# Kernel optimization log

Hardware: AMD Instinct MI355X
Metric: run time of the kernel (lower is better)

Reference implementation:

```python
import jax, jax.numpy as jnp
import numpy as np

N = 50000
E = 800000
NFEAT = 128
NHID = 64
NCLASS = 40


def setup_inputs() -> dict:
    key = jax.random.key(0)
    ks = jax.random.split(key, 12)
    return {
        "x": jax.random.normal(ks[0], (N, NFEAT), dtype=jnp.float32),
        "M": jax.random.uniform(ks[1], (N, 1), dtype=jnp.float32),
        "AM": jax.random.uniform(ks[2], (N, 1), dtype=jnp.float32),
        "adj_vals": jax.random.uniform(ks[3], (E,), dtype=jnp.float32),
        "adjZ_vals": jax.random.uniform(ks[4], (E,), dtype=jnp.float32),
        "W0": jax.random.normal(ks[5], (NFEAT, NFEAT), dtype=jnp.float32) * (1.414 / np.sqrt(NFEAT)),
        "b0": jnp.zeros((NFEAT,), dtype=jnp.float32),
        "W1": jax.random.normal(ks[6], (NFEAT, NHID), dtype=jnp.float32) * (1.414 / np.sqrt(NFEAT)),
        "b1": jnp.zeros((NHID,), dtype=jnp.float32),
        "W2": jax.random.normal(ks[7], (NHID, NCLASS), dtype=jnp.float32) * (1.0 / np.sqrt(NHID)),
        "b2": jnp.zeros((NCLASS,), dtype=jnp.float32),
        "row": jax.random.randint(ks[8], (E,), 0, N, dtype=jnp.int32),
        "col": jax.random.randint(ks[9], (E,), 0, N, dtype=jnp.int32),
    }


def _spmm(vals, row, col, X, n):
    # sparse (COO) @ dense: out[r] = sum_e vals[e] * X[col[e]] for row[e]==r
    return jax.ops.segment_sum(vals[:, None] * X[col], row, num_segments=n)


def reference(x, M, AM, adj_vals, adjZ_vals, W0, b0, W1, b1, W2, b2, row, col):
    n = x.shape[0]
    # gc0: PaGConv(nfeat->nfeat) on adjZ, then ReLU (dropout is identity in eval)
    h = _spmm(adjZ_vals, row, col, M * x, n) * AM
    h = jax.nn.relu(h @ W0 + b0)
    # gc1: PaGConv(nfeat->nhid) on adjZ, then ReLU
    h = _spmm(adjZ_vals, row, col, M * h, n) * AM
    h = jax.nn.relu(h @ W1 + b1)
    # gc2: plain GConv(nhid->nclass) on adj
    h = _spmm(adj_vals, row, col, h, n)
    h = h @ W2 + b2
    return jax.nn.log_softmax(h, axis=1)
```

## Files before the change

kernel.cpp:

```cpp
#include <hip/hip_runtime.h>
#include <hip/hip_bf16.h>
#include <math.h>


typedef __attribute__((ext_vector_type(8))) short bf16x8;
typedef __attribute__((ext_vector_type(4))) float f32x4;

#define HIST_EPB_LOG 14
#define HIST_EPB 16384
#define NBINS 50176
#define NBMAX 50
#define SCAN_BLOCKS 196

__device__ __forceinline__ float rl_f(float v, int j) {
    return __builtin_bit_cast(float,
        __builtin_amdgcn_readlane(__builtin_bit_cast(int, v), j));
}
__device__ __forceinline__ int rl_i(int v, int j) {
    return __builtin_amdgcn_readlane(v, j);
}
__device__ __forceinline__ unsigned short f2bf(float f) {
    unsigned u = __builtin_bit_cast(unsigned, f);
    u += 0x7fffu + ((u >> 16) & 1u);
    return (unsigned short)(u >> 16);
}
__device__ __forceinline__ unsigned pack2bf(float lo, float hi) {
    return (unsigned)f2bf(lo) | ((unsigned)f2bf(hi) << 16);
}
__device__ __forceinline__ float bf_lo(unsigned u) {
    return __builtin_bit_cast(float, u << 16);
}
__device__ __forceinline__ float bf_hi(unsigned u) {
    return __builtin_bit_cast(float, u & 0xffff0000u);
}
__device__ __forceinline__ float clampf(float v) {
    return fminf(fmaxf(v, -1e30f), 1e30f);
}
__device__ __forceinline__ unsigned long long aload(const unsigned long long* p) {
    return __hip_atomic_load(p, __ATOMIC_ACQUIRE, __HIP_MEMORY_SCOPE_AGENT);
}


__global__ void prep_wt(const float* __restrict__ W0, const float* __restrict__ W1,
                        const float* __restrict__ W2,
                        unsigned short* __restrict__ wt0, unsigned short* __restrict__ wt1,
                        unsigned short* __restrict__ wt2,
                        unsigned long long* __restrict__ gpub) {
    if (blockIdx.x == 0) gpub[threadIdx.x] = 0ULL;
    int idx = blockIdx.x * 256 + threadIdx.x;
    if (idx < 128 * 128) {
        int nn = idx >> 7, k = idx & 127;
        wt0[idx] = f2bf(W0[k * 128 + nn]);
    }
    idx -= 128 * 128;
    if (idx >= 0 && idx < 64 * 128) {
        int nn = idx >> 7, k = idx & 127;
        wt1[idx] = f2bf(W1[k * 64 + nn]);
    }
    idx -= 64 * 128;
    if (idx >= 0 && idx < 48 * 64) {
        int nn = idx >> 6, k = idx & 63;
        wt2[idx] = (nn < 40) ? f2bf(W2[k * 40 + nn]) : (unsigned short)0;
    }
}


__launch_bounds__(1024)
__global__ void hist_gemm0(const int* __restrict__ row,
                           unsigned short* __restrict__ cntmat,
                           unsigned short* __restrict__ lrank, int E, int NB,
                           const float* __restrict__ x, const float* __restrict__ Mv,
                           const unsigned short* __restrict__ Wt0,
                           unsigned short* __restrict__ t_buf, int n) {
    __shared__ __align__(16) unsigned hcnt[NBINS / 2];
    const int blk = blockIdx.x;
    const int t = threadIdx.x;
    if (blk < NB) {
        uint4* h4 = (uint4*)hcnt;
        const uint4 z4 = make_uint4(0u, 0u, 0u, 0u);
        for (int i = t; i < NBINS / 8; i += 1024) h4[i] = z4;
        __syncthreads();
        const int s = blk << HIST_EPB_LOG;
        const int e = min(E, s + HIST_EPB);
        for (int i = s + t; i < e; i += 1024) {
            const int r = row[i];
            const unsigned sh = (unsigned)(r & 1) << 4;
            const unsigned old = atomicAdd(&hcnt[r >> 1], 1u << sh);
            lrank[i] = (unsigned short)((old >> sh) & 0xffffu);
        }
        __syncthreads();
        uint4* dst = (uint4*)(cntmat + (size_t)blk * NBINS);
        for (int i = t; i < NBINS / 8; i += 1024) dst[i] = h4[i];
    } else {
        const int tid = t & 255;
        const int bid = (blk - NB) * 4 + (t >> 8);
        const int lane = tid & 63;
        const int wid = tid >> 6;
        const int m15 = lane & 15;
        const int q = lane >> 4;
        const int rA = bid * 64 + wid * 16 + m15;

        bf16x8 a[4];
        {
            float m = 1.0f;
            if (rA < n) m = Mv[rA];
#pragma unroll
            for (int ks = 0; ks < 4; ++ks) {
                float4 lo = make_float4(0.f, 0.f, 0.f, 0.f);
                float4 hi = make_float4(0.f, 0.f, 0.f, 0.f);
                if (rA < n) {
                    lo = *(const float4*)(x + (size_t)rA * 128 + ks * 32 + q * 8);
                    hi = *(const float4*)(x + (size_t)rA * 128 + ks * 32 + q * 8 + 4);
                }
                union { bf16x8 v; unsigned short u[8]; } pk;
                pk.u[0] = f2bf(lo.x * m); pk.u[1] = f2bf(lo.y * m);
                pk.u[2] = f2bf(lo.z * m); pk.u[3] = f2bf(lo.w * m);
                pk.u[4] = f2bf(hi.x * m); pk.u[5] = f2bf(hi.y * m);
                pk.u[6] = f2bf(hi.z * m); pk.u[7] = f2bf(hi.w * m);
                a[ks] = pk.v;
            }
        }
#pragma unroll
        for (int nt = 0; nt < 8; ++nt) {
            f32x4 acc = {0.f, 0.f, 0.f, 0.f};
            const int bn = nt * 16 + m15;
#pragma unroll
            for (int ks = 0; ks < 4; ++ks) {
                const uint4 z = *(const uint4*)(Wt0 + (size_t)bn * 128 + ks * 32 + q * 8);
                acc = __builtin_amdgcn_mfma_f32_16x16x32_bf16(
                    a[ks], __builtin_bit_cast(bf16x8, z), acc, 0, 0, 0);
            }
            const int gc = nt * 16 + m15;
#pragma unroll
            for (int rr = 0; rr < 4; ++rr) {
                const int gr = bid * 64 + wid * 16 + q * 4 + rr;
                if (gr < n) t_buf[(size_t)gr * 128 + gc] = f2bf(clampf(acc[rr]));
            }
        }
    }
}


__launch_bounds__(256)
__global__ void scan_one(const unsigned short* __restrict__ cm,
                         unsigned* __restrict__ cmabs, int* __restrict__ rp,
                         unsigned long long* __restrict__ gpub,
                         int n, int NB, int E) {
    __shared__ int sd[256];
    const int g = blockIdx.x;
    const int t = threadIdx.x;
    const int bin = g * 256 + t;

    unsigned tot = 0;
    for (int b = 0; b < NB; ++b) tot += cm[(size_t)b * NBINS + bin];

    sd[t] = (int)tot;
    __syncthreads();
    for (int off = 1; off < 256; off <<= 1) {
        int xv = (t >= off) ? sd[t - off] : 0;
        __syncthreads();
        sd[t] += xv;
        __syncthreads();
    }
    const int excl = sd[t] - (int)tot;
    const int gtot = sd[255];
    __syncthreads();

    if (t == 0)
        atomicExch(&gpub[g], (1ULL << 32) | (unsigned long long)(unsigned)gtot);

    int my = 0;
    for (int p = t; p < g; p += 256) {
        unsigned long long v;
        do { v = aload(&gpub[p]); } while ((v >> 32) == 0ULL);
        my += (int)(unsigned)v;
    }
    sd[t] = my;
    __syncthreads();
    for (int off = 128; off > 0; off >>= 1) {
        if (t < off) sd[t] += sd[t + off];
        __syncthreads();
    }
    const int base = sd[0];

    const int rpf = base + excl;
    if (bin < n) rp[bin] = rpf;
    if (g == SCAN_BLOCKS - 1 && t == 255) rp[n] = E;

    int run = rpf;
    for (int b = 0; b < NB; ++b) {
        cmabs[(size_t)b * NBINS + bin] = (unsigned)run;
        run += (int)cm[(size_t)b * NBINS + bin];
    }
}


__global__ void scatter_kernel(const int* __restrict__ row, const int* __restrict__ col,
                               const float* __restrict__ vA, const float* __restrict__ vZ,
                               const unsigned* __restrict__ cmabs,
                               const unsigned short* __restrict__ lrank,
                               uint4* __restrict__ packed16, int E) {
    int e = blockIdx.x * blockDim.x + threadIdx.x;
    if (e >= E) return;
    const int r = row[e];
    const int pos = (int)(cmabs[(size_t)(e >> HIST_EPB_LOG) * NBINS + r]
                          + (unsigned)lrank[e]);
    uint4 pk;
    pk.x = (unsigned)col[e];
    pk.y = __builtin_bit_cast(unsigned, vZ[e]);
    pk.z = __builtin_bit_cast(unsigned, vA[e]);
    pk.w = 0u;
    packed16[pos] = pk;
}


__launch_bounds__(256)
__global__ void spmm128_g1(const uint4* __restrict__ packed16,
                           const int* __restrict__ rp, const unsigned short* __restrict__ X,
                           const float* __restrict__ AM, const float* __restrict__ Mv,
                           const float* __restrict__ bias,
                           const unsigned short* __restrict__ wt1,
                           unsigned short* __restrict__ g1, int n) {
    __shared__ __align__(16) unsigned short h16[16][136];
    const int t = threadIdx.x;
    const int lane = t & 63;
    const int w = t >> 6;
    const int rbase = blockIdx.x * 16;

    for (int i = 0; i < 4; ++i) {
        const int lr = w * 4 + i;
        const int r = rbase + lr;
        float o0 = 0.0f, o1 = 0.0f;
        if (r < n) {
            const int s = __builtin_amdgcn_readfirstlane(rp[r]);
            const int e = __builtin_amdgcn_readfirstlane(rp[r + 1]);
            float acc0 = 0.0f, acc1 = 0.0f;
            for (int base = s; base < e; base += 64) {
                const int nn = min(64, e - base);
                int ci = 0; float vf = 0.0f;
                if (lane < nn) {
                    const uint4 pk = packed16[base + lane];
                    ci = (int)pk.x;
                    vf = __builtin_bit_cast(float, pk.y);
                }
                int j = 0;
                for (; j + 16 <= nn; j += 16) {
                    unsigned u[16];
#pragma unroll
                    for (int q = 0; q < 16; ++q) {
                        const int cq = rl_i(ci, j + q);
                        u[q] = *(const unsigned*)(X + (size_t)cq * 128 + lane * 2);
                    }
#pragma unroll
                    for (int q = 0; q < 16; ++q) {
                        const float vq = rl_f(vf, j + q);
                        acc0 += vq * bf_lo(u[q]);
                        acc1 += vq * bf_hi(u[q]);
                    }
                }
                for (; j + 8 <= nn; j += 8) {
                    unsigned u[8];
#pragma unroll
                    for (int q = 0; q < 8; ++q) {
                        const int cq = rl_i(ci, j + q);
                        u[q] = *(const unsigned*)(X + (size_t)cq * 128 + lane * 2);
                    }
#pragma unroll
                    for (int q = 0; q < 8; ++q) {
                        const float vq = rl_f(vf, j + q);
                        acc0 += vq * bf_lo(u[q]);
                        acc1 += vq * bf_hi(u[q]);
                    }
                }
                for (; j < nn; ++j) {
                    const int cq = rl_i(ci, j);
                    const float vq = rl_f(vf, j);
                    const unsigned u = *(const unsigned*)(X + (size_t)cq * 128 + lane * 2);
                    acc0 += vq * bf_lo(u);
                    acc1 += vq * bf_hi(u);
                }
            }
            const float am = AM[r];
            const float mr = Mv[r];
            o0 = fminf(fmaxf((acc0 * am + bias[2 * lane]) * mr, 0.0f), 1e30f);
            o1 = fminf(fmaxf((acc1 * am + bias[2 * lane + 1]) * mr, 0.0f), 1e30f);
        }
        *(unsigned*)&h16[lr][2 * lane] = pack2bf(o0, o1);
    }
    __syncthreads();

    const int m15 = lane & 15;
    const int q = lane >> 4;
    bf16x8 a[4];
#pragma unroll
    for (int ks = 0; ks < 4; ++ks)
        a[ks] = __builtin_bit_cast(bf16x8,
                    *(const uint4*)&h16[m15][ks * 32 + q * 8]);
    f32x4 acc = {0.f, 0.f, 0.f, 0.f};
    const int bn = w * 16 + m15;
#pragma unroll
    for (int ks = 0; ks < 4; ++ks) {
        const uint4 z = *(const uint4*)(wt1 + (size_t)bn * 128 + ks * 32 + q * 8);
        acc = __builtin_amdgcn_mfma_f32_16x16x32_bf16(
            a[ks], __builtin_bit_cast(bf16x8, z), acc, 0, 0, 0);
    }
    const int gcol = w * 16 + m15;
#pragma unroll
    for (int rr = 0; rr < 4; ++rr) {
        const int grow = rbase + q * 4 + rr;
        if (grow < n) g1[(size_t)grow * 64 + gcol] = f2bf(clampf(acc[rr]));
    }
}


__launch_bounds__(256)
__global__ void spmm64_g2(const uint4* __restrict__ packed16,
                          const int* __restrict__ rp, const unsigned short* __restrict__ X,
                          const float* __restrict__ AM, const float* __restrict__ bias1,
                          const unsigned short* __restrict__ wt2,
                          unsigned short* __restrict__ out40, int n) {
    __shared__ __align__(16) unsigned short h16[16][72];
    const int t = threadIdx.x;
    const int lane = t & 63;
    const int w = t >> 6;
    const int g = lane >> 4;
    const int ls = lane & 15;
    const int rbase = blockIdx.x * 16;

    for (int i = 0; i < 4; ++i) {
        const int lr = w * 4 + i;
        const int r = rbase + lr;
        float a0 = 0.0f, a1 = 0.0f, a2 = 0.0f, a3 = 0.0f;
        if (r < n) {
            const int s = __builtin_amdgcn_readfirstlane(rp[r]);
            const int e = __builtin_amdgcn_readfirstlane(rp[r + 1]);
            for (int base = s; base < e; base += 64) {
                const int nn = min(64, e - base);
                int ci = 0; float vf = 0.0f;
                if (lane < nn) {
                    const uint4 pk = packed16[base + lane];
                    ci = (int)pk.x;
                    vf = __builtin_bit_cast(float, pk.y);
                }
                for (int j = 0; j < nn; j += 16) {
#pragma unroll
                    for (int q = 0; q < 4; ++q) {
                        const int jj = j + 4 * q + g;
                        const bool ok = jj < nn;
                        const int idx = jj & 63;
                        const int c = __shfl(ci, idx);
                        const float v = __shfl(vf, idx);
                        if (ok) {
                            const uint2 u = *(const uint2*)(X + (size_t)c * 64 + ls * 4);
                            a0 += v * bf_lo(u.x);
                            a1 += v * bf_hi(u.x);
                            a2 += v * bf_lo(u.y);
                            a3 += v * bf_hi(u.y);
                        }
                    }
                }
            }
            a0 += __shfl_xor(a0, 16); a0 += __shfl_xor(a0, 32);
            a1 += __shfl_xor(a1, 16); a1 += __shfl_xor(a1, 32);
            a2 += __shfl_xor(a2, 16); a2 += __shfl_xor(a2, 32);
            a3 += __shfl_xor(a3, 16); a3 += __shfl_xor(a3, 32);
            const float am = AM[r];
            a0 = fminf(fmaxf(a0 * am + bias1[4 * ls + 0], 0.0f), 1e30f);
            a1 = fminf(fmaxf(a1 * am + bias1[4 * ls + 1], 0.0f), 1e30f);
            a2 = fminf(fmaxf(a2 * am + bias1[4 * ls + 2], 0.0f), 1e30f);
            a3 = fminf(fmaxf(a3 * am + bias1[4 * ls + 3], 0.0f), 1e30f);
        }
        if (lane < 16) {
            uint2 wv;
            wv.x = pack2bf(a0, a1);
            wv.y = pack2bf(a2, a3);
            *(uint2*)&h16[lr][4 * ls] = wv;
        }
    }
    __syncthreads();

    if (w < 3) {
        const int m15 = lane & 15;
        const int q = lane >> 4;
        bf16x8 a[2];
#pragma unroll
        for (int ks = 0; ks < 2; ++ks)
            a[ks] = __builtin_bit_cast(bf16x8,
                        *(const uint4*)&h16[m15][ks * 32 + q * 8]);
        f32x4 acc = {0.f, 0.f, 0.f, 0.f};
        const int bn = w * 16 + m15;
#pragma unroll
        for (int ks = 0; ks < 2; ++ks) {
            const uint4 z = *(const uint4*)(wt2 + (size_t)bn * 64 + ks * 32 + q * 8);
            acc = __builtin_amdgcn_mfma_f32_16x16x32_bf16(
                a[ks], __builtin_bit_cast(bf16x8, z), acc, 0, 0, 0);
        }
        const int gcol = w * 16 + m15;
        if (gcol < 40) {
#pragma unroll
            for (int rr = 0; rr < 4; ++rr) {
                const int grow = rbase + q * 4 + rr;
                if (grow < n) out40[(size_t)grow * 40 + gcol] = f2bf(clampf(acc[rr]));
            }
        }
    }
}


__launch_bounds__(256)
__global__ void spmm40_kernel(const uint4* __restrict__ packed16,
                              const int* __restrict__ rp, const unsigned short* __restrict__ X,
                              const float* __restrict__ bias,
                              float* __restrict__ out, int n) {
    const int lane = threadIdx.x & 63;
    const int g = lane / 20;
    const int ls = lane - 20 * g;
    const bool active = g < 3;
    const int r = (int)((blockIdx.x * (unsigned)blockDim.x + threadIdx.x) >> 6);
    if (r >= n) return;
    const int s = __builtin_amdgcn_readfirstlane(rp[r]);
    const int e = __builtin_amdgcn_readfirstlane(rp[r + 1]);

    float acc0 = 0.0f, acc1 = 0.0f;
    for (int base = s; base < e; base += 64) {
        const int nn = min(64, e - base);
        int ci = 0; float vf = 0.0f;
        if (lane < nn) {
            const uint4 pk = packed16[base + lane];
            ci = (int)pk.x;
            vf = __builtin_bit_cast(float, pk.z);
        }
        for (int j = 0; j < nn; j += 24) {
#pragma unroll
            for (int q = 0; q < 8; ++q) {
                const int jj = j + 3 * q + g;
                const bool ok = active && jj < nn;
                const int idx = jj & 63;
                const int c = __shfl(ci, idx);
                const float v = __shfl(vf, idx);
                if (ok) {
                    const unsigned u = *(const unsigned*)(X + (size_t)c * 40 + ls * 2);
                    acc0 += v * bf_lo(u);
                    acc1 += v * bf_hi(u);
                }
            }
        }
    }
    {
        const float a1 = __shfl(acc0, (lane + 20) & 63);
        const float a2 = __shfl(acc0, (lane + 40) & 63);
        const float b1 = __shfl(acc1, (lane + 20) & 63);
        const float b2 = __shfl(acc1, (lane + 40) & 63);
        acc0 += a1 + a2;
        acc1 += b1 + b2;
    }

    const bool own = lane < 20;
    const float vv0 = own ? fminf(fmaxf(acc0 + bias[2 * ls], -1e30f), 1e30f) : -INFINITY;
    const float vv1 = own ? fminf(fmaxf(acc1 + bias[2 * ls + 1], -1e30f), 1e30f) : -INFINITY;
    float mx = fmaxf(vv0, vv1);
#pragma unroll
    for (int off = 32; off > 0; off >>= 1) mx = fmaxf(mx, __shfl_xor(mx, off));
    float sum = own ? (expf(vv0 - mx) + expf(vv1 - mx)) : 0.0f;
#pragma unroll
    for (int off = 32; off > 0; off >>= 1) sum += __shfl_xor(sum, off);
    if (own) {
        const float lse = mx + logf(sum);
        *(float2*)(out + (size_t)r * 40 + ls * 2) = make_float2(vv0 - lse, vv1 - lse);
    }
}


extern "C" void kernel_launch(void* const* d_in, const int* in_sizes, int n_in,
                              void* d_out, int out_size, void* d_ws, size_t ws_size,
                              hipStream_t stream) {
    const float* x    = (const float*)d_in[0];
    const float* M    = (const float*)d_in[1];
    const float* AM   = (const float*)d_in[2];
    const float* adjv = (const float*)d_in[3];
    const float* adjZ = (const float*)d_in[4];
    const float* W0   = (const float*)d_in[5];
    const float* b0   = (const float*)d_in[6];
    const float* W1   = (const float*)d_in[7];
    const float* b1   = (const float*)d_in[8];
    const float* W2   = (const float*)d_in[9];
    const float* b2   = (const float*)d_in[10];
    const int* row    = (const int*)d_in[11];
    const int* col    = (const int*)d_in[12];
    float* out = (float*)d_out;

    const int n = in_sizes[1];
    const int E = in_sizes[3];

    unsigned short* t_buf = (unsigned short*)d_ws;
    unsigned short* wt0 = t_buf + (size_t)n * 128;
    unsigned short* wt1 = wt0 + 128 * 128;
    unsigned short* wt2 = wt1 + 64 * 128;
    unsigned short* h_buf = wt2 + 48 * 64;
    int* rp = (int*)(h_buf + (size_t)n * 128);
    unsigned long long* gpub = (unsigned long long*)
        (((uintptr_t)(rp + n + 2) + 7) & ~(uintptr_t)7);
    uint4* packed16 = (uint4*)
        (((uintptr_t)(gpub + 256) + 15) & ~(uintptr_t)15);
    unsigned short* lrank = (unsigned short*)(packed16 + (size_t)E);
    unsigned short* cntmat = lrank + (size_t)E;
    unsigned* cmabs = (unsigned*)(cntmat + (size_t)NBMAX * NBINS);

    const int NB = (E + HIST_EPB - 1) >> HIST_EPB_LOG;
    const int gemmBlocks = (n + 63) / 64;
    const int gemmB4 = (gemmBlocks + 3) / 4;

    prep_wt<<<(128 * 128 + 64 * 128 + 48 * 64 + 255) / 256, 256, 0, stream>>>(
        W0, W1, W2, wt0, wt1, wt2, gpub);

    hist_gemm0<<<NB + gemmB4, 1024, 0, stream>>>(row, cntmat, lrank, E, NB,
                                                 x, M, wt0, t_buf, n);

    scan_one<<<SCAN_BLOCKS, 256, 0, stream>>>(cntmat, cmabs, rp, gpub, n, NB, E);

    scatter_kernel<<<(E + 255) / 256, 256, 0, stream>>>(row, col, adjv, adjZ,
                                                        cmabs, lrank, packed16, E);

    const int blk16 = (n + 15) / 16;

    spmm128_g1<<<blk16, 256, 0, stream>>>(packed16, rp, t_buf, AM, M, b0, wt1,
                                          h_buf, n);
    spmm64_g2<<<blk16, 256, 0, stream>>>(packed16, rp, h_buf, AM, b1, wt2,
                                         t_buf, n);
    spmm40_kernel<<<blk16 * 4, 256, 0, stream>>>(packed16, rp, t_buf, b2, out, n);
}
```

Measured before the change: 262.0 us.

## Fold weight prep into hist_gemm0 and reorder scatter blocks by histogram chunk

Removes the separate prep_wt launch. Each GEMM block now converts and transposes W0 into shared memory itself, and an extra block zeroes gpub and prepares wt1/wt2. The scatter grid is remapped so that concurrently running blocks interleave 8 histogram chunks, which changes the locality of cmabs row reads. The aim is to save one launch and cut global weight traffic, at the cost of every GEMM block redundantly converting W0 and adding a __syncthreads.

```diff
diff --git a/kernel.cpp b/kernel.cpp
--- a/kernel.cpp
+++ b/kernel.cpp
@@ -41,37 +41,17 @@
 }
 
 
-__global__ void prep_wt(const float* __restrict__ W0, const float* __restrict__ W1,
-                        const float* __restrict__ W2,
-                        unsigned short* __restrict__ wt0, unsigned short* __restrict__ wt1,
-                        unsigned short* __restrict__ wt2,
-                        unsigned long long* __restrict__ gpub) {
-    if (blockIdx.x == 0) gpub[threadIdx.x] = 0ULL;
-    int idx = blockIdx.x * 256 + threadIdx.x;
-    if (idx < 128 * 128) {
-        int nn = idx >> 7, k = idx & 127;
-        wt0[idx] = f2bf(W0[k * 128 + nn]);
-    }
-    idx -= 128 * 128;
-    if (idx >= 0 && idx < 64 * 128) {
-        int nn = idx >> 7, k = idx & 127;
-        wt1[idx] = f2bf(W1[k * 64 + nn]);
-    }
-    idx -= 64 * 128;
-    if (idx >= 0 && idx < 48 * 64) {
-        int nn = idx >> 6, k = idx & 63;
-        wt2[idx] = (nn < 40) ? f2bf(W2[k * 40 + nn]) : (unsigned short)0;
-    }
-}
-
-
 __launch_bounds__(1024)
 __global__ void hist_gemm0(const int* __restrict__ row,
                            unsigned short* __restrict__ cntmat,
                            unsigned short* __restrict__ lrank, int E, int NB,
                            const float* __restrict__ x, const float* __restrict__ Mv,
-                           const unsigned short* __restrict__ Wt0,
-                           unsigned short* __restrict__ t_buf, int n) {
+                           const float* __restrict__ W0, const float* __restrict__ W1,
+                           const float* __restrict__ W2,
+                           unsigned short* __restrict__ wt1,
+                           unsigned short* __restrict__ wt2,
+                           unsigned long long* __restrict__ gpub,
+                           unsigned short* __restrict__ t_buf, int n, int gemmB4) {
     __shared__ __align__(16) unsigned hcnt[NBINS / 2];
     const int blk = blockIdx.x;
     const int t = threadIdx.x;
@@ -91,7 +71,8 @@
         __syncthreads();
         uint4* dst = (uint4*)(cntmat + (size_t)blk * NBINS);
         for (int i = t; i < NBINS / 8; i += 1024) dst[i] = h4[i];
-    } else {
+    } else if (blk < NB + gemmB4) {
+        unsigned short* w0l = (unsigned short*)hcnt;
         const int tid = t & 255;
         const int bid = (blk - NB) * 4 + (t >> 8);
         const int lane = tid & 63;
@@ -121,12 +102,19 @@
             }
         }
 #pragma unroll
+        for (int i = 0; i < 16; ++i) {
+            const int idx = t + i * 1024;
+            const int k = idx >> 7, nn = idx & 127;
+            w0l[nn * 136 + k] = f2bf(W0[idx]);
+        }
+        __syncthreads();
+#pragma unroll
         for (int nt = 0; nt < 8; ++nt) {
             f32x4 acc = {0.f, 0.f, 0.f, 0.f};
             const int bn = nt * 16 + m15;
 #pragma unroll
             for (int ks = 0; ks < 4; ++ks) {
-                const uint4 z = *(const uint4*)(Wt0 + (size_t)bn * 128 + ks * 32 + q * 8);
+                const uint4 z = *(const uint4*)&w0l[bn * 136 + ks * 32 + q * 8];
                 acc = __builtin_amdgcn_mfma_f32_16x16x32_bf16(
                     a[ks], __builtin_bit_cast(bf16x8, z), acc, 0, 0, 0);
             }
@@ -136,6 +124,16 @@
                 const int gr = bid * 64 + wid * 16 + q * 4 + rr;
                 if (gr < n) t_buf[(size_t)gr * 128 + gc] = f2bf(clampf(acc[rr]));
             }
+        }
+    } else {
+        if (t < 256) gpub[t] = 0ULL;
+        for (int idx = t; idx < 64 * 128; idx += 1024) {
+            int nn = idx >> 7, k = idx & 127;
+            wt1[idx] = f2bf(W1[k * 64 + nn]);
+        }
+        for (int idx = t; idx < 48 * 64; idx += 1024) {
+            int nn = idx >> 6, k = idx & 63;
+            wt2[idx] = (nn < 40) ? f2bf(W2[k * 40 + nn]) : (unsigned short)0;
         }
     }
 }
@@ -195,16 +193,20 @@
 }
 
 
+__launch_bounds__(256)
 __global__ void scatter_kernel(const int* __restrict__ row, const int* __restrict__ col,
                                const float* __restrict__ vA, const float* __restrict__ vZ,
                                const unsigned* __restrict__ cmabs,
                                const unsigned short* __restrict__ lrank,
-                               uint4* __restrict__ packed16, int E) {
-    int e = blockIdx.x * blockDim.x + threadIdx.x;
+                               uint4* __restrict__ packed16, int E, int NB) {
+    const int p = blockIdx.x;
+    const int c = (p & 7) + 8 * (p >> 9);
+    if (c >= NB) return;
+    const int o = (p >> 3) & 63;
+    const int e = (c << HIST_EPB_LOG) + o * 256 + threadIdx.x;
     if (e >= E) return;
     const int r = row[e];
-    const int pos = (int)(cmabs[(size_t)(e >> HIST_EPB_LOG) * NBINS + r]
-                          + (unsigned)lrank[e]);
+    const int pos = (int)(cmabs[(size_t)c * NBINS + r] + (unsigned)lrank[e]);
     uint4 pk;
     pk.x = (unsigned)col[e];
     pk.y = __builtin_bit_cast(unsigned, vZ[e]);
@@ -493,8 +495,7 @@
     const int E = in_sizes[3];
 
     unsigned short* t_buf = (unsigned short*)d_ws;
-    unsigned short* wt0 = t_buf + (size_t)n * 128;
-    unsigned short* wt1 = wt0 + 128 * 128;
+    unsigned short* wt1 = t_buf + (size_t)n * 128;
     unsigned short* wt2 = wt1 + 64 * 128;
     unsigned short* h_buf = wt2 + 48 * 64;
     int* rp = (int*)(h_buf + (size_t)n * 128);
@@ -510,16 +511,16 @@
     const int gemmBlocks = (n + 63) / 64;
     const int gemmB4 = (gemmBlocks + 3) / 4;
 
-    prep_wt<<<(128 * 128 + 64 * 128 + 48 * 64 + 255) / 256, 256, 0, stream>>>(
-        W0, W1, W2, wt0, wt1, wt2, gpub);
-
-    hist_gemm0<<<NB + gemmB4, 1024, 0, stream>>>(row, cntmat, lrank, E, NB,
-                                                 x, M, wt0, t_buf, n);
+    hist_gemm0<<<NB + gemmB4 + 1, 1024, 0, stream>>>(row, cntmat, lrank, E, NB,
+                                                     x, M, W0, W1, W2,
+                                                     wt1, wt2, gpub, t_buf, n,
+                                                     gemmB4);
 
     scan_one<<<SCAN_BLOCKS, 256, 0, stream>>>(cntmat, cmabs, rp, gpub, n, NB, E);
 
-    scatter_kernel<<<(E + 255) / 256, 256, 0, stream>>>(row, col, adjv, adjZ,
-                                                        cmabs, lrank, packed16, E);
+    const int scatGrid = 512 * ((NB + 7) / 8);
+    scatter_kernel<<<scatGrid, 256, 0, stream>>>(row, col, adjv, adjZ,
+                                                 cmabs, lrank, packed16, E, NB);
 
     const int blk16 = (n + 15) / 16;
 
```

Result: faster. 253.2 us (-3.4%).
